# Kernel tuning notes

Measured on AMD Instinct MI355X. Metric: run time of the kernel, lower is better.

The kernel has to match this reference:

```python
import jax, jax.numpy as jnp
import numpy as np

T, B, D_G, D_H, D_OUT = 16, 64, 256, 512, 256
LAMBDA, ETA, S, LN_EPS = 0.95, 0.5, 3, 1e-5


def _ln(x, g, b):
    mu = jnp.mean(x, axis=-1, keepdims=True)
    var = jnp.mean((x - mu) ** 2, axis=-1, keepdims=True)
    return (x - mu) * jax.lax.rsqrt(var + LN_EPS) * g + b


def setup_inputs() -> dict:
    key = jax.random.key(0)
    ks = jax.random.split(key, 6)
    return {
        "z_seq": jax.random.normal(ks[0], (T, B, D_G), jnp.float32),
        "clean_vec": jax.random.normal(ks[1], (B, D_OUT), jnp.float32),
        "W_h": jax.random.normal(ks[2], (D_H, D_H), jnp.float32) * (1.0 / np.sqrt(D_H)),
        "W_g": jax.random.normal(ks[3], (D_H, D_G), jnp.float32) * (1.0 / np.sqrt(D_G)),
        "b_h": jnp.zeros((D_H,), jnp.float32),
        "ln_g": jnp.ones((D_H,), jnp.float32),
        "ln_b": jnp.zeros((D_H,), jnp.float32),
        "alpha_fw": jnp.ones((), jnp.float32),
        "W_head": jax.random.normal(ks[4], (D_OUT, D_H), jnp.float32) * (1.0 / np.sqrt(D_H)),
        "b_head": jnp.zeros((D_OUT,), jnp.float32),
    }


def reference(z_seq, clean_vec, W_h, W_g, b_h, ln_g, ln_b, alpha_fw, W_head, b_head):
    # k = 1 + softplus(alpha) for alpha>=0 else 1/(1+softplus(-alpha))  (compute_k)
    k = jnp.where(alpha_fw >= 0,
                  1.0 + jax.nn.softplus(alpha_fw),
                  1.0 / (1.0 + jax.nn.softplus(-alpha_fw)))

    def base(h, z):
        return h @ W_h.T + z @ W_g.T + b_h

    def step(carry, z_t):  # outer recurrence over t = 0..T-2
        h, A = carry
        h_base = base(h, z_t)                      # [B, d_h]
        h_s = jax.nn.relu(_ln(h_base, ln_g, ln_b))
        for _ in range(S):                          # inner fast-weight settle loop
            Ah = jnp.einsum('bij,bj->bi', A, h_s)   # batched matvec
            dot = jnp.sum(h_s * Ah, axis=-1, keepdims=True)
            n1 = jnp.maximum(jnp.linalg.norm(h_s, axis=-1, keepdims=True), 1e-6)
            n2 = jnp.maximum(jnp.linalg.norm(Ah, axis=-1, keepdims=True), 1e-6)
            R = jnp.clip(dot / (n1 * n2), 0.0, 1.0)
            a = 1.0 - (1.0 - R) ** k                # alpha_dyn
            h_s = jax.nn.relu(_ln((1.0 - a ** 2) * h_base + a * Ah, ln_g, ln_b))
        A = LAMBDA * A + ETA * jnp.einsum('bi,bj->bij', h_s, h_s)  # Hebbian update
        return (h_s, A), None

    Bsz = z_seq.shape[1]
    h0 = jnp.zeros((Bsz, D_H), z_seq.dtype)
    A0 = jnp.zeros((Bsz, D_H, D_H), z_seq.dtype)
    (h, A), _ = jax.lax.scan(step, (h0, A0), z_seq[:-1])

    # final (query) step: plain h_base + Ah inner loop, no alpha blending, no A update
    h_base = base(h, z_seq[-1])
    h = jax.nn.relu(_ln(h_base, ln_g, ln_b))
    for _ in range(S):
        Ah = jnp.einsum('bij,bj->bi', A, h)
        h = jax.nn.relu(_ln(h_base + Ah, ln_g, ln_b))

    pred = h @ W_head.T + b_head
    pred_n = pred / (jnp.linalg.norm(pred, axis=-1, keepdims=True) + 1e-6)
    tgt_n = clean_vec / (jnp.linalg.norm(clean_vec, axis=-1, keepdims=True) + 1e-6)
    loss = jnp.mean((pred_n - tgt_n) ** 2)
    cosine = jnp.mean(jnp.sum(pred_n * tgt_n, axis=-1))
    return loss, cosine
```

## Files before the change

### kernel.cpp

```cpp
#include <hip/hip_runtime.h>
#include <math.h>

#define TT   16
#define BB   64
#define DG   256
#define DH   512
#define DOUT 256

typedef unsigned long long u64t;

__device__ __forceinline__ float dot4(float4 a, float4 b) {
    return fmaf(a.x, b.x, fmaf(a.y, b.y, fmaf(a.z, b.z, a.w * b.w)));
}

__device__ __forceinline__ float blk_sum(float v, float* red, int tid) {
#pragma unroll
    for (int off = 32; off > 0; off >>= 1) v += __shfl_down(v, off, 64);
    if ((tid & 63) == 0) red[tid >> 6] = v;
    __syncthreads();
    float s = ((red[0] + red[1]) + (red[2] + red[3])) +
              ((red[4] + red[5]) + (red[6] + red[7]));
    __syncthreads();
    return s;
}

__device__ __forceinline__ float2 blk_sum2(float a, float b, float* red, int tid) {
#pragma unroll
    for (int off = 32; off > 0; off >>= 1) {
        a += __shfl_down(a, off, 64);
        b += __shfl_down(b, off, 64);
    }
    if ((tid & 63) == 0) { red[tid >> 6] = a; red[8 + (tid >> 6)] = b; }
    __syncthreads();
    float sa = ((red[0] + red[1]) + (red[2] + red[3])) +
               ((red[4] + red[5]) + (red[6] + red[7]));
    float sb = ((red[8] + red[9]) + (red[10] + red[11])) +
               ((red[12] + red[13]) + (red[14] + red[15]));
    __syncthreads();
    return make_float2(sa, sb);
}

__global__ __launch_bounds__(512, 2) void rnn6(
    const float* __restrict__ z,
    const float* __restrict__ clean,
    const float* __restrict__ Wh,
    const float* __restrict__ Wg,
    const float* __restrict__ bh,
    const float* __restrict__ lng,
    const float* __restrict__ lnb,
    const float* __restrict__ alphap,
    const float* __restrict__ Whead,
    const float* __restrict__ bhead,
    u64t* gpart,
    u64t* ssdp, u64t* cosp,
    float* __restrict__ out)
{
    __shared__ __align__(16) float u_lds[(TT - 1) * DH];
    __shared__ __align__(16) float ut[(TT - 1) * DH];
    __shared__ __align__(16) float zp_lds[TT * 128];
    __shared__ __align__(16) float h_lds[DH];
    __shared__ __align__(16) float ht[DH];
    __shared__ __align__(16) float mpart[512];
    __shared__ __align__(16) float ppart[DH];
    __shared__ float red[48];
    __shared__ float d_lds[16];
    __shared__ float cv_lds[16];

    const int tid  = threadIdx.x;
    const int b    = blockIdx.x & 63;
    const int q    = blockIdx.x >> 6;
    const int lane = tid & 63;
    const int wid  = tid >> 6;

    {
        float* z_s = ut;
        for (int f = tid; f < TT * 64; f += 512)
            ((float4*)z_s)[f] = ((const float4*)z)[(size_t)(f >> 6) * (BB * 64) + b * 64 + (f & 63)];
        if (tid < 16) cv_lds[tid] = 0.f;
        __syncthreads();
        const int r  = tid & 127;
        const int tq = tid >> 7;
        const float4* wrow = (const float4*)(Wg + (size_t)((q << 7) + r) * DG);
        float a0 = 0.f, a1 = 0.f, a2 = 0.f, a3 = 0.f;
        for (int j = 0; j < 64; ++j) {
            float4 w = wrow[j];
            a0 += dot4(w, ((const float4*)z_s)[(4 * tq + 0) * 64 + j]);
            a1 += dot4(w, ((const float4*)z_s)[(4 * tq + 1) * 64 + j]);
            a2 += dot4(w, ((const float4*)z_s)[(4 * tq + 2) * 64 + j]);
            a3 += dot4(w, ((const float4*)z_s)[(4 * tq + 3) * 64 + j]);
        }
        float bhr = bh[(q << 7) + r];
        zp_lds[(4 * tq + 0) * 128 + r] = a0 + bhr;
        zp_lds[(4 * tq + 1) * 128 + r] = a1 + bhr;
        zp_lds[(4 * tq + 2) * 128 + r] = a2 + bhr;
        zp_lds[(4 * tq + 3) * 128 + r] = a3 + bhr;
        __syncthreads();
    }

    const float al   = alphap[0];
    const float kexp = (al >= 0.f) ? (1.f + log1pf(expf(al)))
                                   : (1.f / (1.f + log1pf(expf(-al))));
    const float gj = lng[tid];
    const float bj = lnb[tid];

    float wa[128];
    {
        const float* src = Wh + (size_t)((q << 7) + (tid & 127)) * DH + ((tid >> 7) << 7);
#pragma unroll
        for (int k = 0; k < 128; k += 4) {
            float4 v = *(const float4*)(src + k);
            asm volatile("v_accvgpr_write_b32 %0, %1" : "=a"(wa[k + 0]) : "v"(v.x));
            asm volatile("v_accvgpr_write_b32 %0, %1" : "=a"(wa[k + 1]) : "v"(v.y));
            asm volatile("v_accvgpr_write_b32 %0, %1" : "=a"(wa[k + 2]) : "v"(v.z));
            asm volatile("v_accvgpr_write_b32 %0, %1" : "=a"(wa[k + 3]) : "v"(v.w));
        }
    }

    float h = 0.f, hb = 0.f;

#pragma unroll 1
    for (int t = 0; t < TT; ++t) {
        if (t > 0) {
            const int kq = tid >> 7;
            float acc = 0.f;
#pragma unroll
            for (int k4 = 0; k4 < 32; ++k4) {
                float4 h4 = ((const float4*)h_lds)[(kq << 5) + k4];
                float w0, w1, w2, w3;
                asm("v_accvgpr_read_b32 %0, %1" : "=v"(w0) : "a"(wa[4 * k4 + 0]));
                asm("v_accvgpr_read_b32 %0, %1" : "=v"(w1) : "a"(wa[4 * k4 + 1]));
                asm("v_accvgpr_read_b32 %0, %1" : "=v"(w2) : "a"(wa[4 * k4 + 2]));
                asm("v_accvgpr_read_b32 %0, %1" : "=v"(w3) : "a"(wa[4 * k4 + 3]));
                acc = fmaf(w0, h4.x, fmaf(w1, h4.y, fmaf(w2, h4.z, fmaf(w3, h4.w, acc))));
            }
            mpart[tid] = acc;
        }
        __syncthreads();

        const unsigned tag = (unsigned)(t + 1);
        u64t* gb = gpart + ((size_t)(t & 1) * BB + b) * DH;
        if (tid < 128) {
            float m = zp_lds[t * 128 + tid];
            if (t > 0)
                m += (mpart[tid] + mpart[tid + 128]) + (mpart[tid + 256] + mpart[tid + 384]);
            u64t pk = ((u64t)tag << 32) | (u64t)__float_as_uint(m);
            __hip_atomic_store(gb + (q << 7) + tid, pk, __ATOMIC_RELAXED, __HIP_MEMORY_SCOPE_AGENT);
        }
        if (t == TT - 1 && q != 0) return;

        {
            u64t v = __hip_atomic_load(gb + tid, __ATOMIC_RELAXED, __HIP_MEMORY_SCOPE_AGENT);
            while ((unsigned)(v >> 32) != tag) {
                __builtin_amdgcn_s_sleep(1);
                v = __hip_atomic_load(gb + tid, __ATOMIC_RELAXED, __HIP_MEMORY_SCOPE_AGENT);
            }
            hb = __uint_as_float((unsigned)v);
        }

        float S_hb, S_hb2;
        {
            float s1 = hb, s2 = hb * hb;
#pragma unroll
            for (int m = 32; m > 0; m >>= 1) {
                s1 += __shfl_xor(s1, m, 64);
                s2 += __shfl_xor(s2, m, 64);
            }
            if (lane == 0) { red[wid * 2] = s1; red[wid * 2 + 1] = s2; }
            __syncthreads();
            s1 = 0.f; s2 = 0.f;
#pragma unroll
            for (int w = 0; w < 8; ++w) { s1 += red[w * 2]; s2 += red[w * 2 + 1]; }
            S_hb = s1; S_hb2 = s2;
            float mu  = s1 * (1.f / DH);
            float var = s2 * (1.f / DH) - mu * mu;
            h = fmaxf((hb - mu) * rsqrtf(var + 1e-5f) * gj + bj, 0.f);
        }
        ht[(tid & 7) * 64 + (tid >> 3)] = h;
        if (t == 0) {
            h_lds[tid] = h;
            u_lds[tid] = h;
            ut[(tid & 7) * 64 + (tid >> 3)] = h;
        }
        __syncthreads();

        if (t > 0) {
            const bool fin = (t == TT - 1);
            const int  nu  = t;
#pragma unroll 1
            for (int s = 0; s < 3; ++s) {
#pragma unroll
                for (int rep = 0; rep < 2; ++rep) {
                    int i = wid + (rep << 3);
                    if (i < nu) {
                        float a = 0.f;
#pragma unroll
                        for (int k = 0; k < 8; ++k)
                            a = fmaf(ut[i * DH + k * 64 + lane], ht[k * 64 + lane], a);
#pragma unroll
                        for (int m = 32; m > 0; m >>= 1) a += __shfl_xor(a, m, 64);
                        if (lane == 0) d_lds[i] = a * cv_lds[i];
                    }
                }
                __syncthreads();

                float Ah = 0.f;
#pragma unroll
                for (int i = 0; i < TT - 1; ++i)
                    if (i < nu) Ah = fmaf(d_lds[i], u_lds[i * DH + tid], Ah);

                float hAh = h * Ah, AhAh = Ah * Ah, hbAh = hb * Ah, SAh = Ah, hh = h * h;
#pragma unroll
                for (int m = 32; m > 0; m >>= 1) {
                    hAh  += __shfl_xor(hAh,  m, 64);
                    AhAh += __shfl_xor(AhAh, m, 64);
                    hbAh += __shfl_xor(hbAh, m, 64);
                    SAh  += __shfl_xor(SAh,  m, 64);
                    hh   += __shfl_xor(hh,   m, 64);
                }
                if (lane == 0) {
                    red[wid * 5 + 0] = hAh;  red[wid * 5 + 1] = AhAh;
                    red[wid * 5 + 2] = hbAh; red[wid * 5 + 3] = SAh;
                    red[wid * 5 + 4] = hh;
                }
                __syncthreads();
                hAh = 0.f; AhAh = 0.f; hbAh = 0.f; SAh = 0.f; hh = 0.f;
#pragma unroll
                for (int w = 0; w < 8; ++w) {
                    hAh  += red[w * 5 + 0];
                    AhAh += red[w * 5 + 1];
                    hbAh += red[w * 5 + 2];
                    SAh  += red[w * 5 + 3];
                    hh   += red[w * 5 + 4];
                }

                float aa, c1;
                if (!fin) {
                    float n1 = fmaxf(sqrtf(hh),   1e-6f);
                    float n2 = fmaxf(sqrtf(AhAh), 1e-6f);
                    float R  = fminf(fmaxf(hAh / (n1 * n2), 0.f), 1.f);
                    aa = 1.f - __builtin_amdgcn_exp2f(kexp * __builtin_amdgcn_logf(1.f - R));
                    c1 = 1.f - aa * aa;
                } else { aa = 1.f; c1 = 1.f; }

                float Sx   = c1 * S_hb + aa * SAh;
                float Sx2  = c1 * c1 * S_hb2 + 2.f * c1 * aa * hbAh + aa * aa * AhAh;
                float mu2  = Sx * (1.f / DH);
                float var2 = Sx2 * (1.f / DH) - mu2 * mu2;
                float rs2  = rsqrtf(var2 + 1e-5f);
                float x    = c1 * hb + aa * Ah;
                h = fmaxf((x - mu2) * rs2 * gj + bj, 0.f);

                ht[(tid & 7) * 64 + (tid >> 3)] = h;
                if (s == 2) {
                    h_lds[tid] = h;
                    if (!fin) {
                        u_lds[t * DH + tid] = h;
                        ut[t * DH + (tid & 7) * 64 + (tid >> 3)] = h;
                    }
                }
                __syncthreads();
            }
        }
        if (t < TT - 1 && tid < TT - 1) {
            float cvv = cv_lds[tid];
            cv_lds[tid] = (tid < t) ? cvv * 0.95f : (tid == t ? 0.5f : cvv);
        }
    }

    {
        const int oj   = tid & 255;
        const int half = tid >> 8;
        const float4* wr = (const float4*)(Whead + (size_t)oj * DH + half * 256);
        const float4* hv = ((const float4*)h_lds) + half * 64;
        float acc = 0.f;
#pragma unroll 4
        for (int i4 = 0; i4 < 64; ++i4) {
            float4 w  = wr[i4];
            float4 h4 = hv[i4];
            acc += w.x * h4.x + w.y * h4.y + w.z * h4.z + w.w * h4.w;
        }
        ppart[tid] = acc;
        __syncthreads();

        float pred = 0.f, tg = 0.f;
        if (tid < DOUT) {
            pred = ppart[tid] + ppart[tid + 256] + bhead[tid];
            tg   = clean[(size_t)b * DOUT + tid];
        }
        float pss = blk_sum(pred * pred, red, tid);
        float tss = blk_sum(tg * tg, red, tid);
        float pn = pred / (sqrtf(pss) + 1e-6f);
        float tn = tg   / (sqrtf(tss) + 1e-6f);
        float dd = pn - tn;
        float2 lc = blk_sum2(dd * dd, pn * tn, red, tid);
        if (tid == 0) {
            u64t pk = ((u64t)81u << 32) | (u64t)__float_as_uint(lc.x);
            __hip_atomic_store(ssdp + b, pk, __ATOMIC_RELAXED, __HIP_MEMORY_SCOPE_AGENT);
            pk = ((u64t)81u << 32) | (u64t)__float_as_uint(lc.y);
            __hip_atomic_store(cosp + b, pk, __ATOMIC_RELAXED, __HIP_MEMORY_SCOPE_AGENT);
        }
    }

    if (blockIdx.x == 0 && wid == 0) {
        u64t va = __hip_atomic_load(ssdp + lane, __ATOMIC_RELAXED, __HIP_MEMORY_SCOPE_AGENT);
        while ((unsigned)(va >> 32) != 81u) {
            __builtin_amdgcn_s_sleep(1);
            va = __hip_atomic_load(ssdp + lane, __ATOMIC_RELAXED, __HIP_MEMORY_SCOPE_AGENT);
        }
        u64t vc = __hip_atomic_load(cosp + lane, __ATOMIC_RELAXED, __HIP_MEMORY_SCOPE_AGENT);
        while ((unsigned)(vc >> 32) != 81u) {
            __builtin_amdgcn_s_sleep(1);
            vc = __hip_atomic_load(cosp + lane, __ATOMIC_RELAXED, __HIP_MEMORY_SCOPE_AGENT);
        }
        float a = __uint_as_float((unsigned)va);
        float c = __uint_as_float((unsigned)vc);
#pragma unroll
        for (int m = 32; m > 0; m >>= 1) {
            a += __shfl_xor(a, m, 64);
            c += __shfl_xor(c, m, 64);
        }
        if (lane == 0) {
            out[0] = a * (1.f / (BB * DOUT));
            out[1] = c * (1.f / BB);
        }
    }
}

extern "C" void kernel_launch(void* const* d_in, const int* in_sizes, int n_in,
                              void* d_out, int out_size, void* d_ws, size_t ws_size,
                              hipStream_t stream) {
    const float* z     = (const float*)d_in[0];
    const float* clean = (const float*)d_in[1];
    const float* Wh    = (const float*)d_in[2];
    const float* Wg    = (const float*)d_in[3];
    const float* bh    = (const float*)d_in[4];
    const float* lng   = (const float*)d_in[5];
    const float* lnb   = (const float*)d_in[6];
    const float* alpha = (const float*)d_in[7];
    const float* Whead = (const float*)d_in[8];
    const float* bhead = (const float*)d_in[9];
    float* out = (float*)d_out;

    u64t* gpart = (u64t*)d_ws;
    u64t* ssdp  = gpart + (size_t)2 * BB * DH;
    u64t* cosp  = ssdp + BB;

    rnn6<<<4 * BB, 512, 0, stream>>>(z, clean, Wh, Wg, bh, lng, lnb, alpha,
                                     Whead, bhead, gpart, ssdp, cosp, out);
}
```

Before: 252.4 us.

## Compute settle-loop norms from a Gram matrix of stored Hebbian vectors

Result: no change. 256.8 us (+1.7%).

```diff
diff --git a/kernel.cpp b/kernel.cpp
--- a/kernel.cpp
+++ b/kernel.cpp
@@ -40,7 +40,7 @@
     return make_float2(sa, sb);
 }
 
-__global__ __launch_bounds__(512, 2) void rnn6(
+__global__ __launch_bounds__(512, 2) void rnn7(
     const float* __restrict__ z,
     const float* __restrict__ clean,
     const float* __restrict__ Wh,
@@ -56,15 +56,16 @@
     float* __restrict__ out)
 {
     __shared__ __align__(16) float u_lds[(TT - 1) * DH];
-    __shared__ __align__(16) float ut[(TT - 1) * DH];
     __shared__ __align__(16) float zp_lds[TT * 128];
     __shared__ __align__(16) float h_lds[DH];
-    __shared__ __align__(16) float ht[DH];
+    __shared__ __align__(16) float hb_lds[DH];
     __shared__ __align__(16) float mpart[512];
     __shared__ __align__(16) float ppart[DH];
-    __shared__ float red[48];
-    __shared__ float d_lds[16];
-    __shared__ float cv_lds[16];
+    __shared__ float G16[16][16];
+    __shared__ float e_lds[16];
+    __shared__ float f_lds[16];
+    __shared__ float S_lds[16];
+    __shared__ float red[16];
 
     const int tid  = threadIdx.x;
     const int b    = blockIdx.x & 63;
@@ -73,10 +74,9 @@
     const int wid  = tid >> 6;
 
     {
-        float* z_s = ut;
+        float* z_s = u_lds;
         for (int f = tid; f < TT * 64; f += 512)
             ((float4*)z_s)[f] = ((const float4*)z)[(size_t)(f >> 6) * (BB * 64) + b * 64 + (f & 63)];
-        if (tid < 16) cv_lds[tid] = 0.f;
         __syncthreads();
         const int r  = tid & 127;
         const int tq = tid >> 7;
@@ -116,6 +116,10 @@
         }
     }
 
+    float cv[TT - 1];
+#pragma unroll
+    for (int i = 0; i < TT - 1; ++i) cv[i] = 0.f;
+
     float h = 0.f, hb = 0.f;
 
 #pragma unroll 1
@@ -148,16 +152,44 @@
         }
         if (t == TT - 1 && q != 0) return;
 
-        {
-            u64t v = __hip_atomic_load(gb + tid, __ATOMIC_RELAXED, __HIP_MEMORY_SCOPE_AGENT);
-            while ((unsigned)(v >> 32) != tag) {
-                __builtin_amdgcn_s_sleep(1);
-                v = __hip_atomic_load(gb + tid, __ATOMIC_RELAXED, __HIP_MEMORY_SCOPE_AGENT);
-            }
-            hb = __uint_as_float((unsigned)v);
-        }
-
-        float S_hb, S_hb2;
+        u64t v = __hip_atomic_load(gb + tid, __ATOMIC_RELAXED, __HIP_MEMORY_SCOPE_AGENT);
+
+        if (t >= 1) {
+            const float* un = u_lds + (size_t)(t - 1) * DH;
+#pragma unroll
+            for (int rep = 0; rep < 2; ++rep) {
+                int i = wid + (rep << 3);
+                if (i <= t) {
+                    float a = 0.f;
+                    if (i < t) {
+#pragma unroll
+                        for (int k = 0; k < 8; ++k)
+                            a = fmaf(un[k * 64 + lane], u_lds[(size_t)i * DH + k * 64 + lane], a);
+                    } else {
+#pragma unroll
+                        for (int k = 0; k < 8; ++k) a += un[k * 64 + lane];
+                    }
+#pragma unroll
+                    for (int m = 32; m > 0; m >>= 1) a += __shfl_xor(a, m, 64);
+                    if (lane == 0) {
+                        if (i < t) { G16[t - 1][i] = a; G16[i][t - 1] = a; }
+                        else       S_lds[t - 1] = a;
+                    }
+                }
+            }
+        }
+
+        while ((unsigned)(v >> 32) != tag) {
+            __builtin_amdgcn_s_sleep(1);
+            v = __hip_atomic_load(gb + tid, __ATOMIC_RELAXED, __HIP_MEMORY_SCOPE_AGENT);
+        }
+        hb = __uint_as_float((unsigned)v);
+        hb_lds[tid] = hb;
+        __syncthreads();
+
+        const bool fin = (t == TT - 1);
+        const int  nu  = fin ? (TT - 1) : t;
+
         {
             float s1 = hb, s2 = hb * hb;
 #pragma unroll
@@ -166,75 +198,75 @@
                 s2 += __shfl_xor(s2, m, 64);
             }
             if (lane == 0) { red[wid * 2] = s1; red[wid * 2 + 1] = s2; }
-            __syncthreads();
-            s1 = 0.f; s2 = 0.f;
-#pragma unroll
-            for (int w = 0; w < 8; ++w) { s1 += red[w * 2]; s2 += red[w * 2 + 1]; }
-            S_hb = s1; S_hb2 = s2;
-            float mu  = s1 * (1.f / DH);
-            float var = s2 * (1.f / DH) - mu * mu;
+#pragma unroll
+            for (int rep = 0; rep < 2; ++rep) {
+                int i = wid + (rep << 3);
+                if (i < nu) {
+                    float a = 0.f;
+#pragma unroll
+                    for (int k = 0; k < 8; ++k)
+                        a = fmaf(u_lds[(size_t)i * DH + k * 64 + lane], hb_lds[k * 64 + lane], a);
+#pragma unroll
+                    for (int m = 32; m > 0; m >>= 1) a += __shfl_xor(a, m, 64);
+                    if (lane == 0) f_lds[i] = a;
+                }
+            }
+        }
+        __syncthreads();
+
+        float S_hb = 0.f, S_hb2 = 0.f;
+#pragma unroll
+        for (int w = 0; w < 8; ++w) { S_hb += red[w * 2]; S_hb2 += red[w * 2 + 1]; }
+        {
+            float mu  = S_hb * (1.f / DH);
+            float var = S_hb2 * (1.f / DH) - mu * mu;
             h = fmaxf((hb - mu) * rsqrtf(var + 1e-5f) * gj + bj, 0.f);
         }
-        ht[(tid & 7) * 64 + (tid >> 3)] = h;
-        if (t == 0) {
-            h_lds[tid] = h;
-            u_lds[tid] = h;
-            ut[(tid & 7) * 64 + (tid >> 3)] = h;
-        }
+        h_lds[tid] = h;
+        if (t == 0) u_lds[tid] = h;
         __syncthreads();
 
         if (t > 0) {
-            const bool fin = (t == TT - 1);
-            const int  nu  = t;
 #pragma unroll 1
             for (int s = 0; s < 3; ++s) {
 #pragma unroll
                 for (int rep = 0; rep < 2; ++rep) {
                     int i = wid + (rep << 3);
-                    if (i < nu) {
+                    if (i <= nu) {
+                        const float* uv = (i < nu) ? (u_lds + (size_t)i * DH) : h_lds;
                         float a = 0.f;
 #pragma unroll
                         for (int k = 0; k < 8; ++k)
-                            a = fmaf(ut[i * DH + k * 64 + lane], ht[k * 64 + lane], a);
+                            a = fmaf(uv[k * 64 + lane], h_lds[k * 64 + lane], a);
 #pragma unroll
                         for (int m = 32; m > 0; m >>= 1) a += __shfl_xor(a, m, 64);
-                        if (lane == 0) d_lds[i] = a * cv_lds[i];
+                        if (lane == 0) e_lds[i] = a;
                     }
                 }
                 __syncthreads();
 
-                float Ah = 0.f;
-#pragma unroll
-                for (int i = 0; i < TT - 1; ++i)
-                    if (i < nu) Ah = fmaf(d_lds[i], u_lds[i * DH + tid], Ah);
-
-                float hAh = h * Ah, AhAh = Ah * Ah, hbAh = hb * Ah, SAh = Ah, hh = h * h;
-#pragma unroll
-                for (int m = 32; m > 0; m >>= 1) {
-                    hAh  += __shfl_xor(hAh,  m, 64);
-                    AhAh += __shfl_xor(AhAh, m, 64);
-                    hbAh += __shfl_xor(hbAh, m, 64);
-                    SAh  += __shfl_xor(SAh,  m, 64);
-                    hh   += __shfl_xor(hh,   m, 64);
-                }
-                if (lane == 0) {
-                    red[wid * 5 + 0] = hAh;  red[wid * 5 + 1] = AhAh;
-                    red[wid * 5 + 2] = hbAh; red[wid * 5 + 3] = SAh;
-                    red[wid * 5 + 4] = hh;
-                }
-                __syncthreads();
-                hAh = 0.f; AhAh = 0.f; hbAh = 0.f; SAh = 0.f; hh = 0.f;
-#pragma unroll
-                for (int w = 0; w < 8; ++w) {
-                    hAh  += red[w * 5 + 0];
-                    AhAh += red[w * 5 + 1];
-                    hbAh += red[w * 5 + 2];
-                    SAh  += red[w * 5 + 3];
-                    hh   += red[w * 5 + 4];
+                float d[TT - 1];
+#pragma unroll
+                for (int i = 0; i < TT - 1; ++i) d[i] = (i < nu) ? cv[i] * e_lds[i] : 0.f;
+
+                float hAh = 0.f, SAh = 0.f, hbAh = 0.f, AhAh = 0.f;
+#pragma unroll
+                for (int i = 0; i < TT - 1; ++i) {
+                    if (i < nu) {
+                        hAh  = fmaf(d[i], e_lds[i], hAh);
+                        SAh  = fmaf(d[i], S_lds[i], SAh);
+                        hbAh = fmaf(d[i], f_lds[i], hbAh);
+                        float m = d[i] * G16[i][i];
+#pragma unroll
+                        for (int j = 0; j < i; ++j)
+                            m = fmaf(2.f * d[j], G16[i][j], m);
+                        AhAh = fmaf(d[i], m, AhAh);
+                    }
                 }
 
                 float aa, c1;
                 if (!fin) {
+                    float hh = e_lds[nu];
                     float n1 = fmaxf(sqrtf(hh),   1e-6f);
                     float n2 = fmaxf(sqrtf(AhAh), 1e-6f);
                     float R  = fminf(fmaxf(hAh / (n1 * n2), 0.f), 1.f);
@@ -247,23 +279,26 @@
                 float mu2  = Sx * (1.f / DH);
                 float var2 = Sx2 * (1.f / DH) - mu2 * mu2;
                 float rs2  = rsqrtf(var2 + 1e-5f);
-                float x    = c1 * hb + aa * Ah;
+
+                float Ah = 0.f;
+#pragma unroll
+                for (int i = 0; i < TT - 1; ++i)
+                    if (i < nu) Ah = fmaf(d[i], u_lds[(size_t)i * DH + tid], Ah);
+
+                float x = c1 * hb + aa * Ah;
                 h = fmaxf((x - mu2) * rs2 * gj + bj, 0.f);
-
-                ht[(tid & 7) * 64 + (tid >> 3)] = h;
-                if (s == 2) {
-                    h_lds[tid] = h;
-                    if (!fin) {
-                        u_lds[t * DH + tid] = h;
-                        ut[t * DH + (tid & 7) * 64 + (tid >> 3)] = h;
-                    }
-                }
+                h_lds[tid] = h;
+                if (s == 2 && !fin) u_lds[(size_t)t * DH + tid] = h;
                 __syncthreads();
             }
         }
-        if (t < TT - 1 && tid < TT - 1) {
-            float cvv = cv_lds[tid];
-            cv_lds[tid] = (tid < t) ? cvv * 0.95f : (tid == t ? 0.5f : cvv);
+
+        if (t < TT - 1) {
+#pragma unroll
+            for (int i = 0; i < TT - 1; ++i) {
+                if (i < t)       cv[i] *= 0.95f;
+                else if (i == t) cv[i] = 0.5f;
+            }
         }
     }
 
@@ -345,6 +380,6 @@
     u64t* ssdp  = gpart + (size_t)2 * BB * DH;
     u64t* cosp  = ssdp + BB;
 
-    rnn6<<<4 * BB, 512, 0, stream>>>(z, clean, Wh, Wg, bh, lng, lnb, alpha,
+    rnn7<<<4 * BB, 512, 0, stream>>>(z, clean, Wh, Wg, bh, lng, lnb, alpha,
                                      Whead, bhead, gpart, ssdp, cosp, out);
 }
```
